# Optimization experiments

Measured on AMD Instinct MI355X. Metric: run time of the kernel, lower is better.

Reference implementation:

```python
import jax, jax.numpy as jnp
import numpy as np

N_EMBD = 1024
N_HEAD = 16
B, T = 4, 2048


def setup_inputs() -> dict:
    key = jax.random.key(0)
    ks = jax.random.split(key, 4)
    s = 1.0 / np.sqrt(N_EMBD)
    return {
        "x": jax.random.normal(ks[0], (B, T, N_EMBD), dtype=jnp.float32),
        "w_attn": jax.random.normal(ks[1], (N_EMBD, 3 * N_EMBD), dtype=jnp.float32) * s,
        "b_attn": jnp.zeros((3 * N_EMBD,), dtype=jnp.float32),
        "w_proj": jax.random.normal(ks[2], (N_EMBD, N_EMBD), dtype=jnp.float32) * s,
        "b_proj": jnp.zeros((N_EMBD,), dtype=jnp.float32),
    }


def reference(x, w_attn, b_attn, w_proj, b_proj):
    Bb, Tt, C = x.shape
    H = N_HEAD
    D = C // H  # head dim
    qkv = x @ w_attn + b_attn  # [B,T,3C]
    q, k, v = jnp.split(qkv, 3, axis=2)
    # [B,H,T,D]
    q = q.reshape(Bb, Tt, H, D).transpose(0, 2, 1, 3)
    k = k.reshape(Bb, Tt, H, D).transpose(0, 2, 1, 3)
    v = v.reshape(Bb, Tt, H, D).transpose(0, 2, 1, 3)
    scale = 1.0 / np.sqrt(D).astype(np.float32)
    attn = jnp.einsum("bhqd,bhkd->bhqk", q, k) * scale
    mask = jnp.tril(jnp.ones((Tt, Tt), dtype=bool))
    attn = jnp.where(mask, attn, jnp.float32(-jnp.inf))
    probs = jax.nn.softmax(attn, axis=-1)
    out = jnp.einsum("bhqk,bhkd->bhqd", probs, v)
    out = out.transpose(0, 2, 1, 3).reshape(Bb, Tt, C)
    return out @ w_proj + b_proj
```

## Files before the change

### kernel.cpp

```cpp
#include <hip/hip_runtime.h>
#include <hip/hip_bf16.h>


typedef float f32x4 __attribute__((ext_vector_type(4)));
typedef short short8 __attribute__((ext_vector_type(8)));
typedef short short4v __attribute__((ext_vector_type(4)));

__device__ __forceinline__ short f2bf(float f) {
  union { __hip_bfloat16 h; short s; } u;
  u.h = __float2bfloat16(f);
  return u.s;
}

__device__ __forceinline__ void gl_lds16(const void* g, void* l) {
  __builtin_amdgcn_global_load_lds(
      (const __attribute__((address_space(1))) void*)g,
      (__attribute__((address_space(3))) void*)l, 16, 0, 0);
}


__global__ void cvt_f32_bf16(const float* __restrict__ in, short* __restrict__ out) {
  int i = (blockIdx.x * 256 + threadIdx.x) * 4;
  float4 v = *(const float4*)(in + i);
  short4v o;
  o[0] = f2bf(v.x); o[1] = f2bf(v.y); o[2] = f2bf(v.z); o[3] = f2bf(v.w);
  *(short4v*)(out + i) = o;
}

__global__ void transpose_cvt(const float* __restrict__ in, short* __restrict__ out,
                              int K, int N) {
  __shared__ float tile[32][33];
  int bx = blockIdx.x * 32;
  int by = blockIdx.y * 32;
  int tx = threadIdx.x, ty = threadIdx.y;
#pragma unroll
  for (int i = 0; i < 32; i += 8)
    tile[ty + i][tx] = in[(size_t)(by + ty + i) * N + bx + tx];
  __syncthreads();
#pragma unroll
  for (int i = 0; i < 32; i += 8)
    out[(size_t)(bx + ty + i) * K + by + tx] = f2bf(tile[tx][ty + i]);
}

__global__ void transpose_v(const short* __restrict__ in, short* __restrict__ out) {
  __shared__ short tile[32][33];
  const int bh = blockIdx.z;
  const int d0 = blockIdx.x * 32, t0 = blockIdx.y * 32;
  const short* src = in + (size_t)bh * 2048 * 64;
  short* dst = out + (size_t)bh * 64 * 2048;
  int tx = threadIdx.x, ty = threadIdx.y;
#pragma unroll
  for (int i = 0; i < 4; ++i)
    tile[ty + i * 8][tx] = src[(size_t)(t0 + ty + i * 8) * 64 + d0 + tx];
  __syncthreads();
#pragma unroll
  for (int i = 0; i < 4; ++i)
    dst[(size_t)(d0 + ty + i * 8) * 2048 + t0 + tx] = tile[tx][ty + i * 8];
}


#define GEMM_BODY(A_, Bt_)                                                        \
  __shared__ __align__(16) short As[128 * 32];                                    \
  __shared__ __align__(16) short Bs[128 * 32];                                    \
  const int tid = threadIdx.x;                                                    \
  const int wv = tid >> 6;                                                        \
  const int wr = wv >> 1, wc = wv & 1;                                            \
  const int ln = tid & 15, quad = (tid & 63) >> 4;                                \
  const int m0 = blockIdx.y * 128, n0 = blockIdx.x * 128;                         \
  f32x4 acc[4][4];                                                                \
  _Pragma("unroll") for (int i = 0; i < 4; ++i)                                   \
      _Pragma("unroll") for (int j = 0; j < 4; ++j)                               \
          acc[i][j] = (f32x4){0.f, 0.f, 0.f, 0.f};                                \
  for (int k0 = 0; k0 < 1024; k0 += 32) {                                         \
    _Pragma("unroll") for (int i = 0; i < 2; ++i) {                               \
      int cc = tid + i * 256;                                                     \
      int row = cc >> 2, part = cc & 3;                                           \
      gl_lds16(A_ + (size_t)(m0 + row) * 1024 + k0 + part * 8,                    \
               (char*)As + (wv * 64 + i * 256) * 16);                             \
      gl_lds16(Bt_ + (size_t)(n0 + row) * 1024 + k0 + part * 8,                   \
               (char*)Bs + (wv * 64 + i * 256) * 16);                             \
    }                                                                             \
    __syncthreads();                                                              \
    short8 af[4], bf[4];                                                          \
    _Pragma("unroll") for (int i = 0; i < 4; ++i)                                 \
        af[i] = *(const short8*)&As[(wr * 64 + i * 16 + ln) * 32 + quad * 8];     \
    _Pragma("unroll") for (int j = 0; j < 4; ++j)                                 \
        bf[j] = *(const short8*)&Bs[(wc * 64 + j * 16 + ln) * 32 + quad * 8];     \
    _Pragma("unroll") for (int i = 0; i < 4; ++i)                                 \
        _Pragma("unroll") for (int j = 0; j < 4; ++j)                             \
            acc[i][j] =                                                           \
                __builtin_amdgcn_mfma_f32_16x16x32_bf16(af[i], bf[j], acc[i][j],  \
                                                        0, 0, 0);                 \
    __syncthreads();                                                              \
  }

__global__ __launch_bounds__(256, 2) void gemm_qkv(
    const short* __restrict__ A, const short* __restrict__ Bt,
    const float* __restrict__ bias, short* __restrict__ Qb,
    short* __restrict__ Kb, short* __restrict__ Vb) {
  GEMM_BODY(A, Bt)
#pragma unroll
  for (int i = 0; i < 4; ++i) {
#pragma unroll
    for (int j = 0; j < 4; ++j) {
      int n = n0 + wc * 64 + j * 16 + ln;
      int n2 = n & 1023;
      int hh = n2 >> 6, d = n2 & 63;
      float bv = bias[n];
#pragma unroll
      for (int r = 0; r < 4; ++r) {
        int m = m0 + wr * 64 + i * 16 + quad * 4 + r;
        int bb = m >> 11, t = m & 2047;
        float o = acc[i][j][r] + bv;
        size_t idx = ((size_t)((bb << 4) + hh) * 2048 + t) * 64 + d;
        if (n < 1024)
          Qb[idx] = f2bf(o * 0.18033688f);
        else if (n < 2048)
          Kb[idx] = f2bf(o);
        else
          Vb[idx] = f2bf(o);
      }
    }
  }
}

__global__ __launch_bounds__(256, 2) void gemm_proj(
    const short* __restrict__ A, const short* __restrict__ Bt,
    const float* __restrict__ bias, float* __restrict__ out) {
  GEMM_BODY(A, Bt)
#pragma unroll
  for (int i = 0; i < 4; ++i) {
#pragma unroll
    for (int j = 0; j < 4; ++j) {
      int n = n0 + wc * 64 + j * 16 + ln;
      float bv = bias[n];
#pragma unroll
      for (int r = 0; r < 4; ++r) {
        int m = m0 + wr * 64 + i * 16 + quad * 4 + r;
        out[(size_t)m * 1024 + n] = acc[i][j][r] + bv;
      }
    }
  }
}

__global__ __launch_bounds__(256, 2) void flash_attn(
    const short* __restrict__ Qg_, const short* __restrict__ Kg_,
    const short* __restrict__ Vg_, short* __restrict__ Ob) {
  constexpr int STR = 72;
  __shared__ __align__(16) short Kl[2][64 * STR];
  __shared__ __align__(16) short Vl[2][64 * STR];
  const int tid = threadIdx.x;
  const int wv = tid >> 6, ln = tid & 15, quad = (tid & 63) >> 4;
  const int bh = blockIdx.x & 63;
  const int pair = blockIdx.x >> 6;
  const short* Qg = Qg_ + (size_t)bh * 2048 * 64;
  const short* Kg = Kg_ + (size_t)bh * 2048 * 64;
  const short* Vg = Vg_ + (size_t)bh * 64 * 2048;
  const int srow = tid >> 3, spart = tid & 7;
  const int bb = bh >> 4, hh = bh & 15;

  short8 kreg[2], vreg[2];

#define LOADKV(KT)                                                              \
  {                                                                             \
    const short* Kt = Kg + (size_t)(KT) * 64 * 64;                              \
    _Pragma("unroll") for (int i = 0; i < 2; ++i) {                             \
      kreg[i] = *(const short8*)(Kt + (size_t)(srow + i * 32) * 64 + spart * 8);\
      vreg[i] = *(const short8*)(Vg + (size_t)(srow + i * 32) * 2048 +          \
                                 (KT) * 64 + spart * 8);                        \
    }                                                                           \
  }
#define WRITEKV(BUF)                                                            \
  _Pragma("unroll") for (int i = 0; i < 2; ++i) {                               \
    *(short8*)&Kl[BUF][(srow + i * 32) * STR + spart * 8] = kreg[i];            \
    *(short8*)&Vl[BUF][(srow + i * 32) * STR + spart * 8] = vreg[i];            \
  }

#pragma unroll
  for (int it = 0; it < 2; ++it) {
    const int qt = it ? pair : (15 - pair);
    const int q0 = qt * 128;
    const int qbase = q0 + wv * 32;
    const int nkt = (q0 >> 6) + 2;

    short8 qf[2][2];
#pragma unroll
    for (int h = 0; h < 2; ++h)
#pragma unroll
      for (int ch = 0; ch < 2; ++ch)
        qf[h][ch] = *(const short8*)(Qg + (size_t)(qbase + h * 16 + ln) * 64 +
                                     ch * 32 + quad * 8);

    f32x4 Oacc[2][4];
#pragma unroll
    for (int h = 0; h < 2; ++h)
#pragma unroll
      for (int mt = 0; mt < 4; ++mt) Oacc[h][mt] = (f32x4){0.f, 0.f, 0.f, 0.f};
    float lpart[2] = {0.f, 0.f};

    LOADKV(0)
    __syncthreads();
    WRITEKV(0)
    LOADKV(1)

    for (int kt = 0; kt < nkt; ++kt) {
      __syncthreads();
      const short* Kcur = Kl[kt & 1];
      const short* Vcur = Vl[kt & 1];
      if (kt + 1 < nkt) {
        WRITEKV((kt + 1) & 1)
        if (kt + 2 < nkt) LOADKV(kt + 2)
      }

      if (kt * 64 <= qbase + 31) {
        f32x4 St[2][4];
#pragma unroll
        for (int h = 0; h < 2; ++h)
#pragma unroll
          for (int kb = 0; kb < 4; ++kb) St[h][kb] = (f32x4){0.f, 0.f, 0.f, 0.f};
#pragma unroll
        for (int kb = 0; kb < 4; ++kb) {
          short8 ka0 = *(const short8*)&Kcur[(kb * 16 + ln) * STR + quad * 8];
          short8 ka1 = *(const short8*)&Kcur[(kb * 16 + ln) * STR + 32 + quad * 8];
#pragma unroll
          for (int h = 0; h < 2; ++h) {
            St[h][kb] = __builtin_amdgcn_mfma_f32_16x16x32_bf16(
                ka0, qf[h][0], St[h][kb], 0, 0, 0);
            St[h][kb] = __builtin_amdgcn_mfma_f32_16x16x32_bf16(
                ka1, qf[h][1], St[h][kb], 0, 0, 0);
          }
        }

        short4v pf[2][4];
#pragma unroll
        for (int h = 0; h < 2; ++h) {
          const bool needmask = kt * 64 + 63 > qbase + h * 16;
          const int qg = qbase + h * 16 + ln;
#pragma unroll
          for (int kb = 0; kb < 4; ++kb) {
            float p[4];
#pragma unroll
            for (int r = 0; r < 4; ++r) {
              float s = St[h][kb][r];
              if (needmask) {
                int key = kt * 64 + kb * 16 + quad * 4 + r;
                s = (key <= qg) ? s : -1e30f;
              }
              p[r] = __builtin_amdgcn_exp2f(s);
              lpart[h] += p[r];
            }
            union { __hip_bfloat162 b2; unsigned u; } w0, w1;
            w0.b2 = __float22bfloat162_rn(make_float2(p[0], p[1]));
            w1.b2 = __float22bfloat162_rn(make_float2(p[2], p[3]));
            union { short4v s4; unsigned u2[2]; } m;
            m.u2[0] = w0.u; m.u2[1] = w1.u;
            pf[h][kb] = m.s4;
          }
        }

#pragma unroll
        for (int kb = 0; kb < 4; ++kb)
#pragma unroll
          for (int mt = 0; mt < 4; ++mt) {
            short4v va =
                *(const short4v*)&Vcur[(mt * 16 + ln) * STR + kb * 16 + quad * 4];
#pragma unroll
            for (int h = 0; h < 2; ++h)
              Oacc[h][mt] = __builtin_amdgcn_mfma_f32_16x16x16bf16_1k(
                  va, pf[h][kb], Oacc[h][mt], 0, 0, 0);
          }
      }
    }

#pragma unroll
    for (int h = 0; h < 2; ++h) {
      float l = lpart[h];
      l += __shfl_xor(l, 16);
      l += __shfl_xor(l, 32);
      float rl = 1.0f / l;
      int t = qbase + h * 16 + ln;
#pragma unroll
      for (int mt = 0; mt < 4; ++mt) {
        short4v o;
#pragma unroll
        for (int r = 0; r < 4; ++r) o[r] = f2bf(Oacc[h][mt][r] * rl);
        *(short4v*)(Ob + ((size_t)(bb * 2048 + t)) * 1024 + hh * 64 + mt * 16 +
                    quad * 4) = o;
      }
    }
  }
#undef LOADKV
#undef WRITEKV
}


extern "C" void kernel_launch(void* const* d_in, const int* in_sizes, int n_in,
                              void* d_out, int out_size, void* d_ws, size_t ws_size,
                              hipStream_t stream) {
  const float* x      = (const float*)d_in[0];
  const float* w_attn = (const float*)d_in[1];
  const float* b_attn = (const float*)d_in[2];
  const float* w_proj = (const float*)d_in[3];
  const float* b_proj = (const float*)d_in[4];
  float* out = (float*)d_out;
  char* ws = (char*)d_ws;

  short* xb  = (short*)(ws);
  short* wat = (short*)(ws + 16777216);
  short* wpt = (short*)(ws + 23068672);
  short* Qb  = (short*)(ws + 25165824);
  short* Kb  = (short*)(ws + 41943040);
  short* Vtb = (short*)(ws + 58720256);
  short* Ob  = (short*)(ws + 75497472);
  short* Vb  = Ob;

  cvt_f32_bf16<<<8192, 256, 0, stream>>>(x, xb);
  transpose_cvt<<<dim3(96, 32), dim3(32, 8), 0, stream>>>(w_attn, wat, 1024, 3072);
  transpose_cvt<<<dim3(32, 32), dim3(32, 8), 0, stream>>>(w_proj, wpt, 1024, 1024);
  gemm_qkv<<<dim3(24, 64), 256, 0, stream>>>(xb, wat, b_attn, Qb, Kb, Vb);
  transpose_v<<<dim3(2, 64, 64), dim3(32, 8), 0, stream>>>(Vb, Vtb);
  flash_attn<<<512, 256, 0, stream>>>(Qb, Kb, Vtb, Ob);
  gemm_proj<<<dim3(8, 64), 256, 0, stream>>>(Ob, wpt, b_proj, out);
}
```

Before: 269.9 us.

## Fuse prep kernels, use 32x32x16 MFMA, write V transposed from QKV GEMM

Merges the x conversion and both weight transpose-conversions into one prep launch. Switches both GEMMs from 16x16x32 to 32x32x16 bf16 MFMA tiles, which cuts LDS fragment reads per MFMA. The QKV epilogue now writes V directly in transposed layout with 4-element vector stores, removing the separate transpose_v kernel and its extra pass over V. Scattered stores in the epilogue may be less coalesced.

```diff
diff --git a/kernel.cpp b/kernel.cpp
--- a/kernel.cpp
+++ b/kernel.cpp
@@ -3,6 +3,7 @@
 
 
 typedef float f32x4 __attribute__((ext_vector_type(4)));
+typedef float f32x16 __attribute__((ext_vector_type(16)));
 typedef short short8 __attribute__((ext_vector_type(8)));
 typedef short short4v __attribute__((ext_vector_type(4)));
 
@@ -18,44 +19,38 @@
       (__attribute__((address_space(3))) void*)l, 16, 0, 0);
 }
 
-
-__global__ void cvt_f32_bf16(const float* __restrict__ in, short* __restrict__ out) {
-  int i = (blockIdx.x * 256 + threadIdx.x) * 4;
-  float4 v = *(const float4*)(in + i);
-  short4v o;
-  o[0] = f2bf(v.x); o[1] = f2bf(v.y); o[2] = f2bf(v.z); o[3] = f2bf(v.w);
-  *(short4v*)(out + i) = o;
-}
-
-__global__ void transpose_cvt(const float* __restrict__ in, short* __restrict__ out,
-                              int K, int N) {
+__global__ void prep(const float* __restrict__ x, const float* __restrict__ wa,
+                     const float* __restrict__ wp, short* __restrict__ xb,
+                     short* __restrict__ wat, short* __restrict__ wpt) {
+  const int bid = blockIdx.x, tid = threadIdx.x;
+  if (bid < 8192) {
+    int i = (bid * 256 + tid) * 4;
+    float4 v = *(const float4*)(x + i);
+    short4v o;
+    o[0] = f2bf(v.x); o[1] = f2bf(v.y); o[2] = f2bf(v.z); o[3] = f2bf(v.w);
+    *(short4v*)(xb + i) = o;
+    return;
+  }
   __shared__ float tile[32][33];
-  int bx = blockIdx.x * 32;
-  int by = blockIdx.y * 32;
-  int tx = threadIdx.x, ty = threadIdx.y;
+  const float* in;
+  short* out;
+  int N, bx, by;
+  if (bid < 11264) {
+    int t = bid - 8192;
+    in = wa; out = wat; N = 3072; bx = t % 96; by = t / 96;
+  } else {
+    int t = bid - 11264;
+    in = wp; out = wpt; N = 1024; bx = t & 31; by = t >> 5;
+  }
+  int tx = tid & 31, ty = tid >> 5;
+  int x0 = bx * 32, y0 = by * 32;
 #pragma unroll
   for (int i = 0; i < 32; i += 8)
-    tile[ty + i][tx] = in[(size_t)(by + ty + i) * N + bx + tx];
+    tile[ty + i][tx] = in[(size_t)(y0 + ty + i) * N + x0 + tx];
   __syncthreads();
 #pragma unroll
   for (int i = 0; i < 32; i += 8)
-    out[(size_t)(bx + ty + i) * K + by + tx] = f2bf(tile[tx][ty + i]);
-}
-
-__global__ void transpose_v(const short* __restrict__ in, short* __restrict__ out) {
-  __shared__ short tile[32][33];
-  const int bh = blockIdx.z;
-  const int d0 = blockIdx.x * 32, t0 = blockIdx.y * 32;
-  const short* src = in + (size_t)bh * 2048 * 64;
-  short* dst = out + (size_t)bh * 64 * 2048;
-  int tx = threadIdx.x, ty = threadIdx.y;
-#pragma unroll
-  for (int i = 0; i < 4; ++i)
-    tile[ty + i * 8][tx] = src[(size_t)(t0 + ty + i * 8) * 64 + d0 + tx];
-  __syncthreads();
-#pragma unroll
-  for (int i = 0; i < 4; ++i)
-    dst[(size_t)(d0 + ty + i * 8) * 2048 + t0 + tx] = tile[tx][ty + i * 8];
+    out[(size_t)(x0 + ty + i) * 1024 + y0 + tx] = f2bf(tile[tx][ty + i]);
 }
 
 
@@ -65,12 +60,12 @@
   const int tid = threadIdx.x;                                                    \
   const int wv = tid >> 6;                                                        \
   const int wr = wv >> 1, wc = wv & 1;                                            \
-  const int ln = tid & 15, quad = (tid & 63) >> 4;                                \
+  const int col = tid & 31, khalf = (tid >> 5) & 1;                               \
   const int m0 = blockIdx.y * 128, n0 = blockIdx.x * 128;                         \
-  f32x4 acc[4][4];                                                                \
-  _Pragma("unroll") for (int i = 0; i < 4; ++i)                                   \
-      _Pragma("unroll") for (int j = 0; j < 4; ++j)                               \
-          acc[i][j] = (f32x4){0.f, 0.f, 0.f, 0.f};                                \
+  f32x16 acc[2][2];                                                               \
+  _Pragma("unroll") for (int i = 0; i < 2; ++i)                                   \
+      _Pragma("unroll") for (int j = 0; j < 2; ++j)                               \
+          acc[i][j] = (f32x16)(0.f);                                              \
   for (int k0 = 0; k0 < 1024; k0 += 32) {                                         \
     _Pragma("unroll") for (int i = 0; i < 2; ++i) {                               \
       int cc = tid + i * 256;                                                     \
@@ -81,44 +76,60 @@
                (char*)Bs + (wv * 64 + i * 256) * 16);                             \
     }                                                                             \
     __syncthreads();                                                              \
-    short8 af[4], bf[4];                                                          \
-    _Pragma("unroll") for (int i = 0; i < 4; ++i)                                 \
-        af[i] = *(const short8*)&As[(wr * 64 + i * 16 + ln) * 32 + quad * 8];     \
-    _Pragma("unroll") for (int j = 0; j < 4; ++j)                                 \
-        bf[j] = *(const short8*)&Bs[(wc * 64 + j * 16 + ln) * 32 + quad * 8];     \
-    _Pragma("unroll") for (int i = 0; i < 4; ++i)                                 \
-        _Pragma("unroll") for (int j = 0; j < 4; ++j)                             \
-            acc[i][j] =                                                           \
-                __builtin_amdgcn_mfma_f32_16x16x32_bf16(af[i], bf[j], acc[i][j],  \
-                                                        0, 0, 0);                 \
+    short8 af[2][2], bf[2][2];                                                    \
+    _Pragma("unroll") for (int i = 0; i < 2; ++i)                                 \
+        _Pragma("unroll") for (int s = 0; s < 2; ++s) {                           \
+          af[i][s] = *(const short8*)&As[(wr * 64 + i * 32 + col) * 32 +          \
+                                         s * 16 + khalf * 8];                     \
+          bf[i][s] = *(const short8*)&Bs[(wc * 64 + i * 32 + col) * 32 +          \
+                                         s * 16 + khalf * 8];                     \
+        }                                                                         \
+    _Pragma("unroll") for (int s = 0; s < 2; ++s)                                 \
+        _Pragma("unroll") for (int i = 0; i < 2; ++i)                             \
+            _Pragma("unroll") for (int j = 0; j < 2; ++j)                         \
+                acc[i][j] = __builtin_amdgcn_mfma_f32_32x32x16_bf16(              \
+                    af[i][s], bf[j][s], acc[i][j], 0, 0, 0);                      \
     __syncthreads();                                                              \
   }
 
 __global__ __launch_bounds__(256, 2) void gemm_qkv(
     const short* __restrict__ A, const short* __restrict__ Bt,
     const float* __restrict__ bias, short* __restrict__ Qb,
-    short* __restrict__ Kb, short* __restrict__ Vb) {
+    short* __restrict__ Kb, short* __restrict__ Vtb) {
   GEMM_BODY(A, Bt)
-#pragma unroll
-  for (int i = 0; i < 4; ++i) {
-#pragma unroll
-    for (int j = 0; j < 4; ++j) {
-      int n = n0 + wc * 64 + j * 16 + ln;
+  const int rhalf = khalf * 4;
+#pragma unroll
+  for (int i = 0; i < 2; ++i) {
+#pragma unroll
+    for (int j = 0; j < 2; ++j) {
+      int n = n0 + wc * 64 + j * 32 + col;
       int n2 = n & 1023;
       int hh = n2 >> 6, d = n2 & 63;
       float bv = bias[n];
-#pragma unroll
-      for (int r = 0; r < 4; ++r) {
-        int m = m0 + wr * 64 + i * 16 + quad * 4 + r;
-        int bb = m >> 11, t = m & 2047;
-        float o = acc[i][j][r] + bv;
-        size_t idx = ((size_t)((bb << 4) + hh) * 2048 + t) * 64 + d;
-        if (n < 1024)
-          Qb[idx] = f2bf(o * 0.18033688f);
-        else if (n < 2048)
-          Kb[idx] = f2bf(o);
-        else
-          Vb[idx] = f2bf(o);
+      int mb = m0 + wr * 64 + i * 32 + rhalf;
+      int bb = mb >> 11;
+      int bh = (bb << 4) + hh;
+      if (n < 2048) {
+        const bool isq = n < 1024;
+#pragma unroll
+        for (int a = 0; a < 16; ++a) {
+          int t = (mb + (a & 3) + 8 * (a >> 2)) & 2047;
+          float o = acc[i][j][a] + bv;
+          size_t idx = ((size_t)bh * 2048 + t) * 64 + d;
+          if (isq)
+            Qb[idx] = f2bf(o * 0.18033688f);
+          else
+            Kb[idx] = f2bf(o);
+        }
+      } else {
+#pragma unroll
+        for (int g = 0; g < 4; ++g) {
+          int t = (mb + 8 * g) & 2047;
+          short4v o;
+#pragma unroll
+          for (int r = 0; r < 4; ++r) o[r] = f2bf(acc[i][j][g * 4 + r] + bv);
+          *(short4v*)&Vtb[((size_t)bh * 64 + d) * 2048 + t] = o;
+        }
       }
     }
   }
@@ -128,16 +139,18 @@
     const short* __restrict__ A, const short* __restrict__ Bt,
     const float* __restrict__ bias, float* __restrict__ out) {
   GEMM_BODY(A, Bt)
-#pragma unroll
-  for (int i = 0; i < 4; ++i) {
-#pragma unroll
-    for (int j = 0; j < 4; ++j) {
-      int n = n0 + wc * 64 + j * 16 + ln;
+  const int rhalf = khalf * 4;
+#pragma unroll
+  for (int i = 0; i < 2; ++i) {
+#pragma unroll
+    for (int j = 0; j < 2; ++j) {
+      int n = n0 + wc * 64 + j * 32 + col;
       float bv = bias[n];
-#pragma unroll
-      for (int r = 0; r < 4; ++r) {
-        int m = m0 + wr * 64 + i * 16 + quad * 4 + r;
-        out[(size_t)m * 1024 + n] = acc[i][j][r] + bv;
+      int mb = m0 + wr * 64 + i * 32 + rhalf;
+#pragma unroll
+      for (int a = 0; a < 16; ++a) {
+        int m = mb + (a & 3) + 8 * (a >> 2);
+        out[(size_t)m * 1024 + n] = acc[i][j][a] + bv;
       }
     }
   }
@@ -312,13 +325,9 @@
   short* Kb  = (short*)(ws + 41943040);
   short* Vtb = (short*)(ws + 58720256);
   short* Ob  = (short*)(ws + 75497472);
-  short* Vb  = Ob;
-
-  cvt_f32_bf16<<<8192, 256, 0, stream>>>(x, xb);
-  transpose_cvt<<<dim3(96, 32), dim3(32, 8), 0, stream>>>(w_attn, wat, 1024, 3072);
-  transpose_cvt<<<dim3(32, 32), dim3(32, 8), 0, stream>>>(w_proj, wpt, 1024, 1024);
-  gemm_qkv<<<dim3(24, 64), 256, 0, stream>>>(xb, wat, b_attn, Qb, Kb, Vb);
-  transpose_v<<<dim3(2, 64, 64), dim3(32, 8), 0, stream>>>(Vb, Vtb);
+
+  prep<<<12288, 256, 0, stream>>>(x, w_attn, w_proj, xb, wat, wpt);
+  gemm_qkv<<<dim3(24, 64), 256, 0, stream>>>(xb, wat, b_attn, Qb, Kb, Vtb);
   flash_attn<<<512, 256, 0, stream>>>(Qb, Kb, Vtb, Ob);
   gemm_proj<<<dim3(8, 64), 256, 0, stream>>>(Ob, wpt, b_proj, out);
 }
```

Result: no change. 273.3 us (+1.2%).
